# Performance work log

Measured on AMD Instinct MI355X. Metric: run time of the kernel, lower is better.

## Reference

```python
import jax, jax.numpy as jnp
import numpy as np

G = 32        # grid points per axis (in_p is a regular [0,1]^3 grid)
M = 8         # half n_modes (n_modes=16 -> keep 8 low + 8 high per dim, 8 in rfft dim)
NL = 4        # fno_n_layers
HID = 64      # fno_hidden_channels
LIFT = 256    # fno_lifting_channels
NOUT = 16384  # number of output query points
RADIUS = 0.033


def setup_inputs() -> dict:
    key = jax.random.key(0)
    ks = jax.random.split(key, 16)
    g = jnp.linspace(0.0, 1.0, G)
    X, Y, Z = jnp.meshgrid(g, g, g, indexing='ij')
    in_p = jnp.stack([X, Y, Z], -1).astype(jnp.float32)            # [G,G,G,3]
    f = jax.random.normal(ks[0], (G, G, G, 3), jnp.float32)        # [G,G,G,3]
    out_p = jax.random.uniform(ks[1], (NOUT, 3), dtype=jnp.float32)

    def lin(k, i, o):
        return jax.random.normal(k, (i, o), jnp.float32) * (float(i) ** -0.5)

    inp = {
        'in_p': in_p, 'out_p': out_p, 'f': f,
        # Lifting MLP: (in_channels+3)=6 -> 256 -> 64
        'lift_w1': lin(ks[2], 6, LIFT), 'lift_b1': jnp.zeros((LIFT,), jnp.float32),
        'lift_w2': lin(ks[3], LIFT, HID), 'lift_b2': jnp.zeros((HID,), jnp.float32),
        # Spectral weights: [layer, corner(4), in, out, M, M, M, (re,im)]
        'spec_w': jax.random.normal(ks[4], (NL, 4, HID, HID, M, M, M, 2), jnp.float32) * 0.02,
        # Linear (soft) skip per layer
        'skip_w': jax.random.normal(ks[5], (NL, HID, HID), jnp.float32) * (float(HID) ** -0.5),
        'skip_b': jnp.zeros((NL, HID), jnp.float32),
        # GNO kernel MLP: 6 -> 512 -> 256 -> 64
        'gno_w1': lin(ks[6], 6, 512), 'gno_b1': jnp.zeros((512,), jnp.float32),
        'gno_w2': lin(ks[7], 512, 256), 'gno_b2': jnp.zeros((256,), jnp.float32),
        'gno_w3': lin(ks[8], 256, HID), 'gno_b3': jnp.zeros((HID,), jnp.float32),
        # Projection: 64 -> 256 -> 1
        'proj_w1': lin(ks[9], HID, 256), 'proj_b1': jnp.zeros((256,), jnp.float32),
        'proj_w2': lin(ks[10], 256, 1), 'proj_b2': jnp.zeros((1,), jnp.float32),
    }
    return inp


def reference(in_p, out_p, f, lift_w1, lift_b1, lift_w2, lift_b2, spec_w,
              skip_w, skip_b, gno_w1, gno_b1, gno_w2, gno_b2, gno_w3, gno_b3,
              proj_w1, proj_b1, proj_w2, proj_b2):
    gelu = lambda x: jax.nn.gelu(x, approximate=False)

    # ---- FNO latent embedding (channels-last) ----
    h = jnp.concatenate([f, in_p], -1)                               # [G,G,G,6]
    h = gelu(h @ lift_w1 + lift_b1) @ lift_w2 + lift_b2              # [G,G,G,HID]

    w = spec_w[..., 0] + 1j * spec_w[..., 1]                         # [NL,4,i,o,M,M,M]
    lo, hi = slice(0, M), slice(-M, None)
    corners = [(lo, lo), (lo, hi), (hi, lo), (hi, hi)]
    sz = slice(0, M)
    for l in range(NL):
        ft = jnp.fft.rfftn(h, axes=(0, 1, 2), norm='forward')        # [G,G,G//2+1,HID]
        out_ft = jnp.zeros_like(ft)
        for c, (sx, sy) in enumerate(corners):
            blk = jnp.einsum('xyzi,ioxyz->xyzo', ft[sx, sy, sz], w[l, c])
            out_ft = out_ft.at[sx, sy, sz].set(blk)
        hs = jnp.fft.irfftn(out_ft, s=(G, G, G), axes=(0, 1, 2), norm='forward')
        h = hs + h @ skip_w[l] + skip_b[l]
        if l < NL - 1:
            h = gelu(h)
    latent = h.reshape(-1, HID)                                      # [G^3, HID]

    # ---- GNO: radius neighbor search on regular grid + gather-MLP-mean ----
    hgrid = 1.0 / (G - 1)
    i0 = jnp.round(out_p * (G - 1)).astype(jnp.int32)                # nearest cell [N,3]
    off = jnp.stack(jnp.meshgrid(*([jnp.arange(-1, 2)] * 3), indexing='ij'), -1).reshape(-1, 3)
    cand = i0[:, None, :] + off[None]                                # [N,27,3]
    inb = jnp.all((cand >= 0) & (cand < G), -1)
    cc = jnp.clip(cand, 0, G - 1)
    flat = (cc[..., 0] * G + cc[..., 1]) * G + cc[..., 2]            # [N,27]
    ycoord = cc.astype(jnp.float32) * hgrid                          # neighbor coords
    d2 = jnp.sum((out_p[:, None, :] - ycoord) ** 2, -1)
    mask = inb & (d2 <= RADIUS * RADIUS)

    # kernel input = cat([y_coords, x_coords]) per edge -> MLP -> k(x,y) [N,27,HID]
    agg = jnp.concatenate([ycoord, jnp.broadcast_to(out_p[:, None, :], ycoord.shape)], -1)
    k = gelu(agg @ gno_w1 + gno_b1)
    k = gelu(k @ gno_w2 + gno_b2)
    k = k @ gno_w3 + gno_b3
    fy = latent[flat]                                                # gather [N,27,HID]
    msk = mask[..., None].astype(k.dtype)
    num = jnp.sum(k * fy * msk, axis=1)
    den = jnp.maximum(jnp.sum(msk, axis=1), 1.0)
    out = num / den                                                  # [N,HID] (mean reduce)

    # ---- Projection ----
    out = gelu(out @ proj_w1 + proj_b1) @ proj_w2 + proj_b2          # [N,1]
    return out
```

## Files before the change

kernel.cpp:

```cpp
#include <hip/hip_runtime.h>
#include <math.h>


typedef _Float16 f16x8 __attribute__((ext_vector_type(8)));
typedef float f32x4 __attribute__((ext_vector_type(4)));

__device__ __forceinline__ float gelu_f(float x) {
    float t = fabsf(x) * 0.7071067811865475f;
    float k = __builtin_amdgcn_rcpf(1.0f + 0.3275911f * t);
    float e = __expf(-t * t);
    float y = k*(0.254829592f + k*(-0.284496736f + k*(1.421413741f +
              k*(-1.453152027f + k*1.061405429f))));
    float erfv = 1.0f - y * e;
    return 0.5f * x * (1.0f + copysignf(erfv, x));
}

__global__ __launch_bounds__(256) void k_prep_w(const float* __restrict__ w2,
                                                const float* __restrict__ w3,
                                                const float* __restrict__ w1,
                                                const float* __restrict__ b1,
                                                const float* __restrict__ lw2,
                                                _Float16* __restrict__ w2T,
                                                _Float16* __restrict__ w3T,
                                                _Float16* __restrict__ w1p,
                                                _Float16* __restrict__ l2hi,
                                                _Float16* __restrict__ l2lo)
{
    int idx = blockIdx.x*256 + threadIdx.x;
    if (idx < 131072) {
        int k = idx >> 8, n = idx & 255;
        w2T[n*512 + k] = (_Float16)w2[idx];
    } else if (idx < 147456) {
        int j = idx - 131072;
        int k = j >> 6, o = j & 63;
        w3T[o*256 + k] = (_Float16)w3[j];
    } else if (idx < 151552) {
        int j = idx - 147456;
        int k = j >> 3, d = j & 7;
        float v = d < 6 ? w1[d*512 + k] : (d == 6 ? b1[k] : 0.0f);
        w1p[k*8 + d] = (_Float16)v;
    } else if (idx < 167936) {
        int j = idx - 151552;
        int o = j >> 8, k = j & 255;
        float v = lw2[k*64 + o];
        _Float16 hi = (_Float16)v;
        l2hi[j] = hi;
        l2lo[j] = (_Float16)(v - (float)hi);
    }
}

__global__ __launch_bounds__(256) void k_lift(
    const float* __restrict__ f, const float* __restrict__ in_p,
    const float* __restrict__ w1, const float* __restrict__ b1,
    const _Float16* __restrict__ l2hi,
    const _Float16* __restrict__ l2lo,
    const float* __restrict__ b2,
    float* __restrict__ h)
{
    __shared__ __align__(16) _Float16 h1hi[64*264];
    __shared__ __align__(16) _Float16 h1lo[64*264];
    __shared__ float w1s[6*256];
    __shared__ float b1s[256];
    float* oT = (float*)h1hi;
    int t = threadIdx.x;
    for (int i = t; i < 1536; i += 256) w1s[i] = w1[i];
    b1s[t] = b1[t];
    int p0 = blockIdx.x * 64;
    int pt = t >> 2, jq = t & 3;
    int p = p0 + pt;
    float x0 = f[p*3+0], x1 = f[p*3+1], x2 = f[p*3+2];
    float x3 = in_p[p*3+0], x4 = in_p[p*3+1], x5 = in_p[p*3+2];
    __syncthreads();
    for (int r = 0; r < 8; ++r) {
        int j0 = jq*64 + r*8;
        f16x8 vh, vl;
        #pragma unroll
        for (int jj = 0; jj < 8; ++jj) {
            int j = j0 + jj;
            float a = b1s[j] + x0*w1s[j] + x1*w1s[256+j] + x2*w1s[512+j]
                    + x3*w1s[768+j] + x4*w1s[1024+j] + x5*w1s[1280+j];
            float g = gelu_f(a);
            _Float16 hi = (_Float16)g;
            vh[jj] = hi;
            vl[jj] = (_Float16)(g - (float)hi);
        }
        *(f16x8*)&h1hi[pt*264 + j0] = vh;
        *(f16x8*)&h1lo[pt*264 + j0] = vl;
    }
    __syncthreads();
    int w = t >> 6, lane = t & 63, l15 = lane & 15, g = lane >> 4;
    f32x4 acc[4];
    #pragma unroll
    for (int nt = 0; nt < 4; ++nt) {
        float bb = b2[nt*16 + l15];
        acc[nt] = (f32x4){bb, bb, bb, bb};
    }
    for (int kk = 0; kk < 8; ++kk) {
        f16x8 ah = *(const f16x8*)&h1hi[(w*16+l15)*264 + kk*32 + g*8];
        f16x8 al = *(const f16x8*)&h1lo[(w*16+l15)*264 + kk*32 + g*8];
        #pragma unroll
        for (int nt = 0; nt < 4; ++nt) {
            f16x8 bh = *(const f16x8*)&l2hi[(nt*16+l15)*256 + kk*32 + g*8];
            f16x8 bl = *(const f16x8*)&l2lo[(nt*16+l15)*256 + kk*32 + g*8];
            acc[nt] = __builtin_amdgcn_mfma_f32_16x16x32_f16(al, bh, acc[nt], 0, 0, 0);
            acc[nt] = __builtin_amdgcn_mfma_f32_16x16x32_f16(ah, bl, acc[nt], 0, 0, 0);
            acc[nt] = __builtin_amdgcn_mfma_f32_16x16x32_f16(ah, bh, acc[nt], 0, 0, 0);
        }
    }
    __syncthreads();
    #pragma unroll
    for (int nt = 0; nt < 4; ++nt)
        #pragma unroll
        for (int r = 0; r < 4; ++r)
            oT[(nt*16 + l15)*68 + w*16 + g*4 + r] = acc[nt][r];
    __syncthreads();
    for (int i = t; i < 4096; i += 256) {
        int c = i >> 6, ptl = i & 63;
        h[(size_t)c*32768 + p0 + ptl] = oT[c*68 + ptl];
    }
}

__global__ __launch_bounds__(256) void k_fwd_zy(const float* __restrict__ h,
                                                float2* __restrict__ F1)
{
    __shared__ float pl[8*1056];
    __shared__ float2 fz[32*73];
    __shared__ float twc[32], tws[32];
    int t = threadIdx.x;
    int x = blockIdx.x >> 3, cg = blockIdx.x & 7;
    for (int i = t; i < 8192; i += 256) {
        int c = i >> 10, yz = i & 1023;
        pl[c*1056 + (yz>>5)*33 + (yz&31)] = h[(cg*8 + c)*32768 + x*1024 + yz];
    }
    if (t < 32) { float th = (float)t*(6.283185307179586f/32.f); twc[t]=cosf(th); tws[t]=sinf(th); }
    __syncthreads();
    {
        int c = t >> 5, y = t & 31;
        float zv[32];
        #pragma unroll
        for (int z = 0; z < 32; ++z) zv[z] = pl[c*1056 + y*33 + z];
        const float inv = 1.0f/32768.0f;
        #pragma unroll
        for (int kz = 0; kz < 8; ++kz) {
            float re = 0.f, im = 0.f;
            #pragma unroll
            for (int z = 0; z < 32; ++z) {
                int ph = (kz*z)&31;
                re += zv[z]*twc[ph];
                im -= zv[z]*tws[ph];
            }
            fz[y*73 + kz*9 + c] = make_float2(re*inv, im*inv);
        }
    }
    __syncthreads();
    #pragma unroll
    for (int ko = 0; ko < 4; ++ko) {
        int idx = ko*256 + t;
        int kyi = idx >> 6, kz = (idx >> 3) & 7, c = idx & 7;
        int ky = kyi < 8 ? kyi : kyi + 16;
        float re = 0.f, im = 0.f;
        for (int y = 0; y < 32; ++y) {
            int ph = (ky*y)&31;
            float cc = twc[ph], ss = tws[ph];
            float2 a = fz[y*73 + kz*9 + c];
            re += a.x*cc + a.y*ss;
            im += a.y*cc - a.x*ss;
        }
        F1[((kyi*8 + kz)*32 + x)*64 + cg*8 + c] = make_float2(re, im);
    }
}

__global__ __launch_bounds__(256) void k_fwd_x(const float2* __restrict__ F1,
                                               float2* __restrict__ Ft)
{
    __shared__ float2 fs[32*65];
    __shared__ float twc[32], tws[32];
    int t = threadIdx.x;
    int kyi = blockIdx.x >> 3, kz = blockIdx.x & 7;
    const float2* src = &F1[(size_t)((kyi*8 + kz)*32)*64];
    for (int i = t; i < 2048; i += 256) fs[(i>>6)*65 + (i&63)] = src[i];
    if (t < 32) { float th = (float)t*(6.283185307179586f/32.f); twc[t]=cosf(th); tws[t]=sinf(th); }
    __syncthreads();
    #pragma unroll
    for (int ko = 0; ko < 4; ++ko) {
        int idx = ko*256 + t;
        int kxi = idx >> 6, ii = idx & 63;
        int kx = kxi < 8 ? kxi : kxi + 16;
        float re = 0.f, im = 0.f;
        for (int xx = 0; xx < 32; ++xx) {
            int ph = (kx*xx)&31;
            float cc = twc[ph], ss = tws[ph];
            float2 a = fs[xx*65 + ii];
            re += a.x*cc + a.y*ss;
            im += a.y*cc - a.x*ss;
        }
        Ft[((kxi*16 + kyi)*8 + kz)*64 + ii] = make_float2(re, im);
    }
}

__global__ __launch_bounds__(256) void k_spec(const float2* __restrict__ Ft,
                                              const float* __restrict__ spw,
                                              float2* __restrict__ Gt, int l)
{
    __shared__ float2 ft[64*65];
    int t = threadIdx.x;
    int og = blockIdx.x >> 5, corner = (blockIdx.x >> 3) & 3, mx = blockIdx.x & 7;
    int kxi = mx + (corner >> 1)*8;
    int kyB = (corner & 1)*8;
    {
        int m = t >> 2, iq = t & 3;
        int my = m >> 3, mz = m & 7;
        const float2* src = &Ft[(size_t)((kxi*16 + kyB + my)*8 + mz)*64];
        #pragma unroll
        for (int ii = 0; ii < 16; ++ii) {
            int i = iq*16 + ii;
            ft[i*65 + m] = src[i];
        }
    }
    __syncthreads();
    int mode = t & 63, o = t >> 6;
    size_t wbase = (size_t)(l*4 + corner)*4194304 + (size_t)(og*4 + o)*1024
                 + (size_t)mx*128 + mode*2;
    float ar = 0.f, ai = 0.f;
    for (int i8 = 0; i8 < 64; i8 += 8) {
        float2 wv[8];
        #pragma unroll
        for (int u = 0; u < 8; ++u)
            wv[u] = *(const float2*)&spw[wbase + (size_t)(i8+u)*65536];
        #pragma unroll
        for (int u = 0; u < 8; ++u) {
            float2 fv = ft[(i8+u)*65 + mode];
            ar += fv.x*wv[u].x - fv.y*wv[u].y;
            ai += fv.x*wv[u].y + fv.y*wv[u].x;
        }
    }
    Gt[(size_t)(((og*4 + corner)*8 + mx)*64 + mode)*4 + o] = make_float2(ar, ai);
}

__global__ __launch_bounds__(256) void k_inv_skip(const float2* __restrict__ Gt,
                                                  const float* __restrict__ hold,
                                                  const float* __restrict__ skw,
                                                  const float* __restrict__ skb,
                                                  float* __restrict__ hnew,
                                                  float* __restrict__ latent,
                                                  int l)
{
    __shared__ float2 gt[8192];
    __shared__ float2 s1[16*8*4];
    __shared__ float2 s2[32*8*4];
    __shared__ float  skws[256];
    __shared__ float twc[32], tws[32];
    int t = threadIdx.x;
    int x = blockIdx.x >> 4, og = blockIdx.x & 15;
    const float2* gsrc = &Gt[(size_t)og*8192];
    for (int i = t; i < 8192; i += 256) gt[i] = gsrc[i];
    skws[t] = skw[l*4096 + (t>>2)*64 + og*4 + (t&3)];
    if (t < 32) { float th = (float)t*(6.283185307179586f/32.f); twc[t]=cosf(th); tws[t]=sinf(th); }
    __syncthreads();
    #pragma unroll
    for (int ko = 0; ko < 2; ++ko) {
        int idx = ko*256 + t;
        int kyi = idx >> 5, kz = (idx >> 2) & 7, o = idx & 3;
        int cy = kyi >> 3, my = kyi & 7;
        float re = 0.f, im = 0.f;
        #pragma unroll
        for (int cxh = 0; cxh < 2; ++cxh) {
            int corner = cxh*2 + cy;
            #pragma unroll
            for (int mxx = 0; mxx < 8; ++mxx) {
                int kxi = cxh*8 + mxx;
                int kx = kxi < 8 ? kxi : kxi + 16;
                int ph = (kx * x) & 31;
                float cc = twc[ph], ss = tws[ph];
                float2 a = gt[((corner*8 + mxx)*64 + my*8 + kz)*4 + o];
                re += a.x*cc - a.y*ss;
                im += a.x*ss + a.y*cc;
            }
        }
        s1[(kyi*8 + kz)*4 + o] = make_float2(re, im);
    }
    __syncthreads();
    #pragma unroll
    for (int ko = 0; ko < 4; ++ko) {
        int idx = ko*256 + t;
        int y = idx >> 5, kz = (idx >> 2) & 7, o = idx & 3;
        float re = 0.f, im = 0.f;
        #pragma unroll
        for (int kyi = 0; kyi < 16; ++kyi) {
            int ky = kyi < 8 ? kyi : kyi + 16;
            int ph = (ky*y) & 31;
            float cc = twc[ph], ss = tws[ph];
            float2 a = s1[(kyi*8 + kz)*4 + o];
            re += a.x*cc - a.y*ss;
            im += a.x*ss + a.y*cc;
        }
        s2[(y*8 + kz)*4 + o] = make_float2(re, im);
    }
    __syncthreads();
    float acc[4][4];
    #pragma unroll
    for (int pp = 0; pp < 4; ++pp)
        #pragma unroll
        for (int o = 0; o < 4; ++o) acc[pp][o] = skb[l*64 + og*4 + o];
    const float* hsrc = &hold[x*1024 + t*4];
    for (int i = 0; i < 64; ++i) {
        float4 hv = *(const float4*)&hsrc[(size_t)i*32768];
        #pragma unroll
        for (int o = 0; o < 4; ++o) {
            float wv = skws[i*4 + o];
            acc[0][o] += hv.x*wv; acc[1][o] += hv.y*wv;
            acc[2][o] += hv.z*wv; acc[3][o] += hv.w*wv;
        }
    }
    float outv[4][4];
    #pragma unroll
    for (int pp = 0; pp < 4; ++pp) {
        int pt = t*4 + pp;
        int y = pt >> 5, z = pt & 31;
        #pragma unroll
        for (int o = 0; o < 4; ++o) {
            float s = s2[(y*8)*4 + o].x;
            #pragma unroll
            for (int kz = 1; kz < 8; ++kz) {
                int ph = (kz*z) & 31;
                float2 a = s2[(y*8 + kz)*4 + o];
                s += 2.0f*(a.x*twc[ph] - a.y*tws[ph]);
            }
            float v = s + acc[pp][o];
            outv[pp][o] = (l < 3) ? gelu_f(v) : v;
        }
    }
    if (l < 3) {
        #pragma unroll
        for (int o = 0; o < 4; ++o) {
            float4 w4 = make_float4(outv[0][o], outv[1][o], outv[2][o], outv[3][o]);
            *(float4*)&hnew[(size_t)(og*4 + o)*32768 + x*1024 + t*4] = w4;
        }
    } else {
        #pragma unroll
        for (int pp = 0; pp < 4; ++pp) {
            float4 w4 = make_float4(outv[pp][0], outv[pp][1], outv[pp][2], outv[pp][3]);
            *(float4*)&latent[(size_t)(x*1024 + t*4 + pp)*64 + og*4] = w4;
        }
    }
}

__global__ __launch_bounds__(256, 2) void k_gno(
    const float* __restrict__ out_p,
    const _Float16* __restrict__ w1p,
    const _Float16* __restrict__ w2T,
    const float* __restrict__ b2,
    const _Float16* __restrict__ w3T,
    const float* __restrict__ b3,
    const float* __restrict__ latent,
    float* __restrict__ num)
{
    __shared__ __align__(16) _Float16 h1pool[64*520];
    __shared__ __align__(16) _Float16 w1s[512*8];
    __shared__ int   flatS[64];
    __shared__ float validS[64];
    __shared__ float cntS[8];
    _Float16* h2h = h1pool;

    int t = threadIdx.x;
    const float hg = 1.0f/31.0f;
    const float r2 = (float)(0.033*0.033);

    for (int i = t; i < 512; i += 256)
        ((int4*)w1s)[i] = ((const int4*)w1p)[i];

    int e = t & 63;
    int p = blockIdx.x*8 + (e >> 3);
    int slot = e & 7;
    float px = out_p[p*3+0], py = out_p[p*3+1], pz = out_p[p*3+2];
    int ix = (int)rintf(px*31.f), iy = (int)rintf(py*31.f), iz = (int)rintf(pz*31.f);
    int found = -1, cnt = 0;
    for (int j = 0; j < 27; ++j) {
        int dx = j/9 - 1, dy = (j/3)%3 - 1, dz = j%3 - 1;
        int cx = ix+dx, cy = iy+dy, cz = iz+dz;
        bool inb = (cx>=0)&&(cx<32)&&(cy>=0)&&(cy<32)&&(cz>=0)&&(cz<32);
        int qx = min(max(cx,0),31), qy = min(max(cy,0),31), qz = min(max(cz,0),31);
        float yx = qx*hg, yy = qy*hg, yz = qz*hg;
        float d2 = (px-yx)*(px-yx) + (py-yy)*(py-yy) + (pz-yz)*(pz-yz);
        if (inb && d2 <= r2) { if (cnt == slot) found = j; cnt++; }
    }
    float a0=0.f,a1=0.f,a2=0.f,a3=0.f,a4=0.f,a5=0.f;
    int fl = 0; float val = 0.f;
    if (found >= 0) {
        int dx = found/9 - 1, dy = (found/3)%3 - 1, dz = found%3 - 1;
        int cx = ix+dx, cy = iy+dy, cz = iz+dz;
        fl = (cx*32 + cy)*32 + cz;
        a0 = cx*hg; a1 = cy*hg; a2 = cz*hg; a3 = px; a4 = py; a5 = pz;
        val = 1.f;
    }
    if (t < 64) {
        flatS[e] = fl; validS[e] = val;
        if (slot == 0) cntS[e >> 3] = (float)cnt;
    }
    __syncthreads();

    int w = t >> 6;
    {
        int xk = (e >> 3) & 7;
        #pragma unroll
        for (int ci = 0; ci < 16; ++ci) {
            int c = w*16 + ci;
            f16x8 v;
            #pragma unroll
            for (int jj = 0; jj < 8; ++jj) {
                int k = c*8 + jj;
                f16x8 wv = *(const f16x8*)&w1s[k*8];
                float pre = (float)wv[6]
                    + a0*(float)wv[0] + a1*(float)wv[1] + a2*(float)wv[2]
                    + a3*(float)wv[3] + a4*(float)wv[4] + a5*(float)wv[5];
                v[jj] = (_Float16)gelu_f(pre);
            }
            *(f16x8*)&h1pool[e*520 + ((c ^ xk)*8)] = v;
        }
    }
    __syncthreads();

    int lane = t & 63;
    int l15 = lane & 15, g = lane >> 4;

    f32x4 acc2[4][4];
    #pragma unroll
    for (int nt = 0; nt < 4; ++nt) {
        float bb = b2[w*64 + nt*16 + l15];
        #pragma unroll
        for (int mt = 0; mt < 4; ++mt) acc2[mt][nt] = (f32x4){bb, bb, bb, bb};
    }
    #pragma unroll 4
    for (int kk = 0; kk < 16; ++kk) {
        f16x8 af[4];
        #pragma unroll
        for (int mt = 0; mt < 4; ++mt) {
            int ee = mt*16 + l15;
            af[mt] = *(const f16x8*)&h1pool[ee*520 + (((kk*4 + g) ^ ((ee>>3)&7))*8)];
        }
        #pragma unroll
        for (int nt = 0; nt < 4; ++nt) {
            f16x8 bf = *(const f16x8*)&w2T[(size_t)(w*64 + nt*16 + l15)*512 + kk*32 + g*8];
            #pragma unroll
            for (int mt = 0; mt < 4; ++mt)
                acc2[mt][nt] = __builtin_amdgcn_mfma_f32_16x16x32_f16(af[mt], bf, acc2[mt][nt], 0, 0, 0);
        }
    }
    __syncthreads();
    #pragma unroll
    for (int mt = 0; mt < 4; ++mt)
      #pragma unroll
      for (int nt = 0; nt < 4; ++nt) {
        int n = w*64 + nt*16 + l15;
        #pragma unroll
        for (int r = 0; r < 4; ++r) {
            int m = mt*16 + g*4 + r;
            h2h[m*264 + (((n>>3) ^ (m&7))*8) + (n&7)] = (_Float16)gelu_f(acc2[mt][nt][r]);
        }
      }
    __syncthreads();

    int o = w*16 + l15;
    f32x4 acc3[4];
    { float bb = b3[o];
      #pragma unroll
      for (int mt = 0; mt < 4; ++mt) acc3[mt] = (f32x4){bb, bb, bb, bb}; }
    #pragma unroll 2
    for (int kk2 = 0; kk2 < 8; ++kk2) {
        f16x8 bf = *(const f16x8*)&w3T[(size_t)o*256 + kk2*32 + g*8];
        #pragma unroll
        for (int mt = 0; mt < 4; ++mt) {
            int ee = mt*16 + l15;
            f16x8 af = *(const f16x8*)&h2h[ee*264 + (((kk2*4 + g) ^ (ee&7))*8)];
            acc3[mt] = __builtin_amdgcn_mfma_f32_16x16x32_f16(af, bf, acc3[mt], 0, 0, 0);
        }
    }

    #pragma unroll
    for (int mt = 0; mt < 4; ++mt) {
        float psum = 0.f;
        #pragma unroll
        for (int r = 0; r < 4; ++r) {
            int ee = mt*16 + g*4 + r;
            float fy = latent[(size_t)flatS[ee]*64 + o];
            psum += acc3[mt][r] * fy * validS[ee];
        }
        psum += __shfl_xor(psum, 16, 64);
        if ((g & 1) == 0) {
            int pt = mt*2 + (g >> 1);
            float den = fmaxf(cntS[pt], 1.0f);
            num[(size_t)(blockIdx.x*8 + pt)*64 + o] = psum / den;
        }
    }
}

__global__ __launch_bounds__(256) void k_project(const float* __restrict__ num,
                                                 const float* __restrict__ pw1,
                                                 const float* __restrict__ pb1,
                                                 const float* __restrict__ pw2,
                                                 const float* __restrict__ pb2,
                                                 float* __restrict__ outp)
{
    __shared__ float w1s[64*260];
    __shared__ float xT[64*68];
    __shared__ float w2s[256];
    __shared__ float b1s[256];
    __shared__ float red[64*4];
    int t = threadIdx.x;
    int p0 = blockIdx.x * 64;
    for (int i = t; i < 16384; i += 256) {
        int k = i >> 8, o = i & 255;
        w1s[k*260 + o] = pw1[i];
    }
    w2s[t] = pw2[t];
    b1s[t] = pb1[t];
    for (int i = t; i < 4096; i += 256) {
        int ptl = i >> 6, c = i & 63;
        xT[c*68 + ptl] = num[(size_t)(p0 + ptl)*64 + c];
    }
    __syncthreads();
    int pr = t & 15, oc0 = t >> 4;
    float psum[4] = {0.f, 0.f, 0.f, 0.f};
    for (int it = 0; it < 4; ++it) {
        int oc = it*16 + oc0;
        float a[4][4];
        #pragma unroll
        for (int pp = 0; pp < 4; ++pp)
            #pragma unroll
            for (int q = 0; q < 4; ++q) a[pp][q] = b1s[oc*4 + q];
        for (int i = 0; i < 64; ++i) {
            float4 xv = *(const float4*)&xT[i*68 + pr*4];
            float4 wv = *(const float4*)&w1s[i*260 + oc*4];
            #pragma unroll
            for (int q = 0; q < 4; ++q) {
                float wq = (&wv.x)[q];
                a[0][q] += xv.x*wq; a[1][q] += xv.y*wq;
                a[2][q] += xv.z*wq; a[3][q] += xv.w*wq;
            }
        }
        #pragma unroll
        for (int pp = 0; pp < 4; ++pp) {
            float s = 0.f;
            #pragma unroll
            for (int q = 0; q < 4; ++q) s += gelu_f(a[pp][q]) * w2s[oc*4 + q];
            psum[pp] += s;
        }
    }
    #pragma unroll
    for (int pp = 0; pp < 4; ++pp) {
        psum[pp] += __shfl_xor(psum[pp], 16, 64);
        psum[pp] += __shfl_xor(psum[pp], 32, 64);
    }
    int lane = t & 63, w = t >> 6;
    if (lane < 16) {
        #pragma unroll
        for (int pp = 0; pp < 4; ++pp) red[(lane*4 + pp)*4 + w] = psum[pp];
    }
    __syncthreads();
    if (t < 64)
        outp[p0 + t] = red[t*4+0] + red[t*4+1] + red[t*4+2] + red[t*4+3] + pb2[0];
}

extern "C" void kernel_launch(void* const* d_in, const int* in_sizes, int n_in,
                              void* d_out, int out_size, void* d_ws, size_t ws_size,
                              hipStream_t stream)
{
    const float* in_p = (const float*)d_in[0];
    const float* outp = (const float*)d_in[1];
    const float* f    = (const float*)d_in[2];
    const float* lw1  = (const float*)d_in[3];
    const float* lb1  = (const float*)d_in[4];
    const float* lw2  = (const float*)d_in[5];
    const float* lb2  = (const float*)d_in[6];
    const float* spw  = (const float*)d_in[7];
    const float* skw  = (const float*)d_in[8];
    const float* skb  = (const float*)d_in[9];
    const float* gw1  = (const float*)d_in[10];
    const float* gb1  = (const float*)d_in[11];
    const float* gw2  = (const float*)d_in[12];
    const float* gb2  = (const float*)d_in[13];
    const float* gw3  = (const float*)d_in[14];
    const float* gb3  = (const float*)d_in[15];
    const float* pw1  = (const float*)d_in[16];
    const float* pb1  = (const float*)d_in[17];
    const float* pw2  = (const float*)d_in[18];
    const float* pb2  = (const float*)d_in[19];

    float* ws   = (float*)d_ws;
    float* buf0 = ws;
    float* buf1 = ws + 2097152;
    float* SC   = ws + 4194304;
    float2* F1 = (float2*)SC;
    float2* Ft = (float2*)(SC + 524288);
    float2* Gt = (float2*)(SC + 786432);
    float* numb = SC;
    _Float16* w2T  = (_Float16*)(SC + 1048576);
    _Float16* w3T  = (_Float16*)(SC + 1114112);
    _Float16* w1p  = (_Float16*)(SC + 1122304);
    _Float16* l2hi = (_Float16*)(SC + 1124352);
    _Float16* l2lo = (_Float16*)(SC + 1132544);

    k_prep_w<<<656, 256, 0, stream>>>(gw2, gw3, gw1, gb1, lw2,
                                      w2T, w3T, w1p, l2hi, l2lo);
    k_lift<<<512, 256, 0, stream>>>(f, in_p, lw1, lb1, l2hi, l2lo, lb2, buf0);

    for (int l = 0; l < 4; ++l) {
        const float* hin = (l & 1) ? buf1 : buf0;
        float* hout = (l & 1) ? buf0 : buf1;
        k_fwd_zy<<<256, 256, 0, stream>>>(hin, F1);
        k_fwd_x<<<128, 256, 0, stream>>>(F1, Ft);
        k_spec<<<512, 256, 0, stream>>>(Ft, spw, Gt, l);
        k_inv_skip<<<512, 256, 0, stream>>>(Gt, hin, skw, skb, hout, buf0, l);
    }

    k_gno<<<2048, 256, 0, stream>>>(outp, w1p, w2T, gb2, w3T, gb3, buf0, numb);
    k_project<<<256, 256, 0, stream>>>(numb, pw1, pb1, pw2, pb2, (float*)d_out);
}
```

Baseline: 430.2 us.

## Compact GNO edges into a dense list and widen spectral mixing per thread

The GNO stage previously gave each query point 8 fixed edge slots, so the kernel MLP also ran on masked-out slots. A build kernel now collects the valid neighbor edges into a compact list using an atomic counter. An MLP kernel then processes only those edges, and a reduce kernel averages them per point. In exchange it adds two kernel launches, a memset, intermediate global buffers and a fixed edge capacity (ECAP) that silently truncates if exceeded. Separately, k_spec now has each thread compute two modes using float4 weight loads, halving the grid.

```diff
diff --git a/kernel.cpp b/kernel.cpp
--- a/kernel.cpp
+++ b/kernel.cpp
@@ -1,6 +1,8 @@
 #include <hip/hip_runtime.h>
 #include <math.h>
 
+
+#define ECAP 131072
 
 typedef _Float16 f16x8 __attribute__((ext_vector_type(8)));
 typedef float f32x4 __attribute__((ext_vector_type(4)));
@@ -202,39 +204,47 @@
                                               const float* __restrict__ spw,
                                               float2* __restrict__ Gt, int l)
 {
-    __shared__ float2 ft[64*65];
-    int t = threadIdx.x;
-    int og = blockIdx.x >> 5, corner = (blockIdx.x >> 3) & 3, mx = blockIdx.x & 7;
+    __shared__ float2 ft2[64*65];
+    int t = threadIdx.x;
+    int og8 = blockIdx.x >> 5, corner = (blockIdx.x >> 3) & 3, mx = blockIdx.x & 7;
     int kxi = mx + (corner >> 1)*8;
     int kyB = (corner & 1)*8;
     {
         int m = t >> 2, iq = t & 3;
         int my = m >> 3, mz = m & 7;
+        int rho = (m >> 1) + ((m & 1) << 5);
         const float2* src = &Ft[(size_t)((kxi*16 + kyB + my)*8 + mz)*64];
         #pragma unroll
         for (int ii = 0; ii < 16; ++ii) {
             int i = iq*16 + ii;
-            ft[i*65 + m] = src[i];
-        }
-    }
-    __syncthreads();
-    int mode = t & 63, o = t >> 6;
-    size_t wbase = (size_t)(l*4 + corner)*4194304 + (size_t)(og*4 + o)*1024
-                 + (size_t)mx*128 + mode*2;
-    float ar = 0.f, ai = 0.f;
+            ft2[rho*65 + i] = src[i];
+        }
+    }
+    __syncthreads();
+    int mp = t & 31, oq = t >> 5;
+    int o = og8*8 + oq;
+    int m0 = 2*mp;
+    size_t wbase = (size_t)(l*4 + corner)*4194304 + (size_t)o*1024
+                 + (size_t)mx*128 + m0*2;
+    float ar0 = 0.f, ai0 = 0.f, ar1 = 0.f, ai1 = 0.f;
     for (int i8 = 0; i8 < 64; i8 += 8) {
-        float2 wv[8];
+        float4 wv[8];
         #pragma unroll
         for (int u = 0; u < 8; ++u)
-            wv[u] = *(const float2*)&spw[wbase + (size_t)(i8+u)*65536];
+            wv[u] = *(const float4*)&spw[wbase + (size_t)(i8+u)*65536];
         #pragma unroll
         for (int u = 0; u < 8; ++u) {
-            float2 fv = ft[(i8+u)*65 + mode];
-            ar += fv.x*wv[u].x - fv.y*wv[u].y;
-            ai += fv.x*wv[u].y + fv.y*wv[u].x;
-        }
-    }
-    Gt[(size_t)(((og*4 + corner)*8 + mx)*64 + mode)*4 + o] = make_float2(ar, ai);
+            float2 f0 = ft2[mp*65 + i8 + u];
+            float2 f1 = ft2[(32 + mp)*65 + i8 + u];
+            ar0 += f0.x*wv[u].x - f0.y*wv[u].y;
+            ai0 += f0.x*wv[u].y + f0.y*wv[u].x;
+            ar1 += f1.x*wv[u].z - f1.y*wv[u].w;
+            ai1 += f1.x*wv[u].w + f1.y*wv[u].z;
+        }
+    }
+    size_t gbase = (size_t)(o >> 2)*8192 + (size_t)(corner*8 + mx)*256 + (o & 3);
+    Gt[gbase + (size_t)m0*4]       = make_float2(ar0, ai0);
+    Gt[gbase + (size_t)(m0+1)*4]   = make_float2(ar1, ai1);
 }
 
 __global__ __launch_bounds__(256) void k_inv_skip(const float2* __restrict__ Gt,
@@ -345,36 +355,19 @@
     }
 }
 
-__global__ __launch_bounds__(256, 2) void k_gno(
-    const float* __restrict__ out_p,
-    const _Float16* __restrict__ w1p,
-    const _Float16* __restrict__ w2T,
-    const float* __restrict__ b2,
-    const _Float16* __restrict__ w3T,
-    const float* __restrict__ b3,
-    const float* __restrict__ latent,
-    float* __restrict__ num)
-{
-    __shared__ __align__(16) _Float16 h1pool[64*520];
-    __shared__ __align__(16) _Float16 w1s[512*8];
-    __shared__ int   flatS[64];
-    __shared__ float validS[64];
-    __shared__ float cntS[8];
-    _Float16* h2h = h1pool;
-
-    int t = threadIdx.x;
+__global__ __launch_bounds__(256) void k_gno_build(const float* __restrict__ out_p,
+                                                   int* __restrict__ counter,
+                                                   int* __restrict__ baseG,
+                                                   int* __restrict__ cntG,
+                                                   int* __restrict__ eFlat,
+                                                   float* __restrict__ eAgg)
+{
+    int n = blockIdx.x*256 + threadIdx.x;
     const float hg = 1.0f/31.0f;
     const float r2 = (float)(0.033*0.033);
-
-    for (int i = t; i < 512; i += 256)
-        ((int4*)w1s)[i] = ((const int4*)w1p)[i];
-
-    int e = t & 63;
-    int p = blockIdx.x*8 + (e >> 3);
-    int slot = e & 7;
-    float px = out_p[p*3+0], py = out_p[p*3+1], pz = out_p[p*3+2];
+    float px = out_p[n*3+0], py = out_p[n*3+1], pz = out_p[n*3+2];
     int ix = (int)rintf(px*31.f), iy = (int)rintf(py*31.f), iz = (int)rintf(pz*31.f);
-    int found = -1, cnt = 0;
+    unsigned msk = 0; int cnt = 0;
     for (int j = 0; j < 27; ++j) {
         int dx = j/9 - 1, dy = (j/3)%3 - 1, dz = j%3 - 1;
         int cx = ix+dx, cy = iy+dy, cz = iz+dz;
@@ -382,25 +375,58 @@
         int qx = min(max(cx,0),31), qy = min(max(cy,0),31), qz = min(max(cz,0),31);
         float yx = qx*hg, yy = qy*hg, yz = qz*hg;
         float d2 = (px-yx)*(px-yx) + (py-yy)*(py-yy) + (pz-yz)*(pz-yz);
-        if (inb && d2 <= r2) { if (cnt == slot) found = j; cnt++; }
-    }
-    float a0=0.f,a1=0.f,a2=0.f,a3=0.f,a4=0.f,a5=0.f;
-    int fl = 0; float val = 0.f;
-    if (found >= 0) {
-        int dx = found/9 - 1, dy = (found/3)%3 - 1, dz = found%3 - 1;
+        if (inb && d2 <= r2) { msk |= 1u<<j; cnt++; }
+    }
+    int base = atomicAdd(counter, cnt);
+    baseG[n] = base; cntG[n] = cnt;
+    int k = 0;
+    for (int j = 0; j < 27; ++j) if (msk & (1u<<j)) {
+        int dx = j/9 - 1, dy = (j/3)%3 - 1, dz = j%3 - 1;
         int cx = ix+dx, cy = iy+dy, cz = iz+dz;
-        fl = (cx*32 + cy)*32 + cz;
-        a0 = cx*hg; a1 = cy*hg; a2 = cz*hg; a3 = px; a4 = py; a5 = pz;
-        val = 1.f;
-    }
-    if (t < 64) {
-        flatS[e] = fl; validS[e] = val;
-        if (slot == 0) cntS[e >> 3] = (float)cnt;
-    }
-    __syncthreads();
-
+        int e = base + k;
+        eFlat[e] = (cx*32 + cy)*32 + cz;
+        eAgg[e*6+0] = cx*hg; eAgg[e*6+1] = cy*hg; eAgg[e*6+2] = cz*hg;
+        eAgg[e*6+3] = px;    eAgg[e*6+4] = py;    eAgg[e*6+5] = pz;
+        ++k;
+    }
+}
+
+__global__ __launch_bounds__(256, 2) void k_gno_mlp(
+    const int* __restrict__ counter,
+    const int* __restrict__ eFlat,
+    const float* __restrict__ eAgg,
+    const _Float16* __restrict__ w1p,
+    const _Float16* __restrict__ w2T,
+    const float* __restrict__ b2,
+    const _Float16* __restrict__ w3T,
+    const float* __restrict__ b3,
+    const float* __restrict__ latent,
+    float* __restrict__ kv)
+{
+    __shared__ __align__(16) _Float16 h1pool[64*520];
+    __shared__ __align__(16) _Float16 w1s[512*8];
+    __shared__ float aggs[64][6];
+    __shared__ int   flatS[64];
+    _Float16* h2h = h1pool;
+
+    int t = threadIdx.x;
+    int E = counter[0]; if (E > ECAP) E = ECAP;
+    int s = blockIdx.x * 64;
+    if (s >= E) return;
+    int ne = min(64, E - s);
+
+    for (int i = t; i < 512; i += 256)
+        ((int4*)w1s)[i] = ((const int4*)w1p)[i];
+    for (int i = t; i < 384; i += 256)
+        aggs[i/6][i - (i/6)*6] = (i < ne*6) ? eAgg[(size_t)s*6 + i] : 0.0f;
+    if (t < 64) flatS[t] = (t < ne) ? eFlat[s + t] : 0;
+    __syncthreads();
+
+    int e = t & 63;
     int w = t >> 6;
     {
+        float a0 = aggs[e][0], a1 = aggs[e][1], a2 = aggs[e][2];
+        float a3 = aggs[e][3], a4 = aggs[e][4], a5 = aggs[e][5];
         int xk = (e >> 3) & 7;
         #pragma unroll
         for (int ci = 0; ci < 16; ++ci) {
@@ -478,20 +504,34 @@
 
     #pragma unroll
     for (int mt = 0; mt < 4; ++mt) {
-        float psum = 0.f;
         #pragma unroll
         for (int r = 0; r < 4; ++r) {
             int ee = mt*16 + g*4 + r;
-            float fy = latent[(size_t)flatS[ee]*64 + o];
-            psum += acc3[mt][r] * fy * validS[ee];
-        }
-        psum += __shfl_xor(psum, 16, 64);
-        if ((g & 1) == 0) {
-            int pt = mt*2 + (g >> 1);
-            float den = fmaxf(cntS[pt], 1.0f);
-            num[(size_t)(blockIdx.x*8 + pt)*64 + o] = psum / den;
-        }
-    }
+            if (ee < ne) {
+                float fy = latent[(size_t)flatS[ee]*64 + o];
+                kv[(size_t)(s + ee)*64 + o] = acc3[mt][r] * fy;
+            }
+        }
+    }
+}
+
+__global__ __launch_bounds__(256) void k_gno_reduce(const int* __restrict__ baseG,
+                                                    const int* __restrict__ cntG,
+                                                    const float* __restrict__ kv,
+                                                    float* __restrict__ num)
+{
+    int t = threadIdx.x;
+    int p = blockIdx.x*16 + (t >> 4);
+    int cg = t & 15;
+    int base = baseG[p], cnt = cntG[p];
+    float4 acc = make_float4(0.f, 0.f, 0.f, 0.f);
+    for (int j = 0; j < cnt; ++j) {
+        float4 v = *(const float4*)&kv[(size_t)(base + j)*64 + cg*4];
+        acc.x += v.x; acc.y += v.y; acc.z += v.z; acc.w += v.w;
+    }
+    float inv = 1.0f / fmaxf((float)cnt, 1.0f);
+    acc.x *= inv; acc.y *= inv; acc.z *= inv; acc.w *= inv;
+    *(float4*)&num[(size_t)p*64 + cg*4] = acc;
 }
 
 __global__ __launch_bounds__(256) void k_project(const float* __restrict__ num,
@@ -599,20 +639,31 @@
     _Float16* w1p  = (_Float16*)(SC + 1122304);
     _Float16* l2hi = (_Float16*)(SC + 1124352);
     _Float16* l2lo = (_Float16*)(SC + 1132544);
+    int*   counter = (int*)(SC + 1140736);
+    int*   baseG   = (int*)(SC + 1140752);
+    int*   cntG    = (int*)(SC + 1157136);
+    int*   eFlat   = (int*)(SC + 1173520);
+    float* eAgg    = SC + 1304592;
+    float* kv      = SC + 2091024;
 
     k_prep_w<<<656, 256, 0, stream>>>(gw2, gw3, gw1, gb1, lw2,
                                       w2T, w3T, w1p, l2hi, l2lo);
     k_lift<<<512, 256, 0, stream>>>(f, in_p, lw1, lb1, l2hi, l2lo, lb2, buf0);
+
+    hipMemsetAsync(counter, 0, sizeof(int), stream);
+    k_gno_build<<<64, 256, 0, stream>>>(outp, counter, baseG, cntG, eFlat, eAgg);
 
     for (int l = 0; l < 4; ++l) {
         const float* hin = (l & 1) ? buf1 : buf0;
         float* hout = (l & 1) ? buf0 : buf1;
         k_fwd_zy<<<256, 256, 0, stream>>>(hin, F1);
         k_fwd_x<<<128, 256, 0, stream>>>(F1, Ft);
-        k_spec<<<512, 256, 0, stream>>>(Ft, spw, Gt, l);
+        k_spec<<<256, 256, 0, stream>>>(Ft, spw, Gt, l);
         k_inv_skip<<<512, 256, 0, stream>>>(Gt, hin, skw, skb, hout, buf0, l);
     }
 
-    k_gno<<<2048, 256, 0, stream>>>(outp, w1p, w2T, gb2, w3T, gb3, buf0, numb);
+    k_gno_mlp<<<ECAP/64, 256, 0, stream>>>(counter, eFlat, eAgg,
+                                           w1p, w2T, gb2, w3T, gb3, buf0, kv);
+    k_gno_reduce<<<1024, 256, 0, stream>>>(baseG, cntG, kv, numb);
     k_project<<<256, 256, 0, stream>>>(numb, pw1, pb1, pw2, pb2, (float*)d_out);
 }
```

Result: faster. 417.6 us (-2.9%).
